# Kernel tuning notes

Hardware: AMD Instinct MI355X
Metric: run time of the kernel (lower is better)

Reference implementation:

```python
import jax, jax.numpy as jnp
import numpy as np

B, I, N, D = 4, 32, 4096, 64
TEM = 1.0
WP = 0.5


def setup_inputs() -> dict:
    key = jax.random.key(0)
    kf, kl = jax.random.split(key)
    x = jax.random.normal(kf, (B, N, D), dtype=jnp.float32)
    # features are L2-normalized ('normed_corr_features')
    x = x / jnp.linalg.norm(x, axis=-1, keepdims=True)
    # assign each correspondence to one of I instances -> boolean masks [B, I, N]
    inst = jax.random.randint(kl, (B, N), 0, I)
    label = (inst[:, None, :] == jnp.arange(I)[None, :, None])  # bool [B, I, N]
    return {"normed_corr_features": x, "label": label}


def reference(normed_corr_features, label):
    x = normed_corr_features                      # [B, N, D]
    m = label.astype(x.dtype)                     # [B, I, N]
    cnt = m.sum(-1)                               # [B, I]
    valid = (cnt >= 5).astype(x.dtype)            # skip instances with <5 points

    sim = jnp.einsum('bpd,bnd->bpn', x, x)        # [B, N, N] full similarity

    # loss_p: mse(sim_p, ones) over the cnt x cnt masked submatrix
    sq = (sim - 1.0) ** 2                         # [B, N, N]
    t = jnp.einsum('bip,bpn->bin', m, sq)         # [B, I, N]
    lp = (t * m).sum(-1) / jnp.maximum(cnt * cnt, 1.0)  # [B, I]

    # loss_n: mean over positive rows p of log(sum over negatives n of exp(sim/tem))
    e = jnp.exp(sim / TEM)                        # [B, N, N]
    s = jnp.einsum('bpn,bin->bip', e, 1.0 - m)    # [B, I, N] row sums over negatives
    ln = (jnp.log(jnp.maximum(s, 1e-30)) * m).sum(-1) / jnp.maximum(cnt, 1.0)  # [B, I]

    denom = jnp.asarray(B * I, x.dtype)
    loss_p = (valid * lp).sum() / denom
    loss_n = (valid * ln).sum() / denom
    return WP * loss_p + (1.0 - WP) * loss_n
```

## Files before the change

### kernel.cpp

```cpp
#include <hip/hip_runtime.h>
#include <stdint.h>

#define Bsz 4
#define Isz 32
#define Nsz 4096
#define Dsz 64
#define WPc 0.5f
#define ALPHA 1.2011224087864498f
#define LN2 0.69314718055994531f
#define LSZ2 256
#define GBLK (Isz * Bsz * 2)

typedef __attribute__((ext_vector_type(8))) short short8;
typedef __attribute__((ext_vector_type(4))) float floatx4;

__device__ inline uint16_t f2bf(float f) {
  uint32_t u = __float_as_uint(f);
  u += 0x7fffu + ((u >> 16) & 1u);
  return (uint16_t)(u >> 16);
}
__device__ inline float exp2_raw(float f) { return __builtin_amdgcn_exp2f(f); }

__device__ inline void load_lds16(const uint16_t* g, void* l) {
  __builtin_amdgcn_global_load_lds(
      (const __attribute__((address_space(1))) uint32_t*)g,
      (__attribute__((address_space(3))) uint32_t*)l, 16, 0, 0);
}

__global__ __launch_bounds__(256) void prep_kernel(
    const float* __restrict__ x, uint16_t* __restrict__ xb,
    float* __restrict__ negtot, float* __restrict__ accum,
    int* __restrict__ ticket) {
  const int t = threadIdx.x;
  const int blk = blockIdx.x;
  const int idx4 = (blk * 256 + t) * 4;
  const float4 v = *(const float4*)(x + idx4);
  ushort4 o;
  o.x = f2bf(v.x * ALPHA);
  o.y = f2bf(v.y * ALPHA);
  o.z = f2bf(v.z * ALPHA);
  o.w = f2bf(v.w * ALPHA);
  *(ushort4*)(xb + idx4) = o;
  if (blk < 64) {
    const int p = blk * 256 + t;
    negtot[p] = 0.f;
    if (p == 0) {
      accum[0] = 0.f;
      ticket[0] = 0;
    }
  }
}

__global__ __launch_bounds__(256) void rowsum4_kernel(
    const uint16_t* __restrict__ xb, float* __restrict__ negtot) {
  __shared__ uint4 sbuf[2][1024];

  const int t = threadIdx.x;
  const int lane = t & 63;
  const int w = t >> 6;
  const int quad = lane >> 4;
  const int l15 = lane & 15;

  const int b = blockIdx.y;
  const int row0 = (blockIdx.x >> 3) * 128;
  const int cg0 = (blockIdx.x & 7) * 512;
  const size_t bN = (size_t)b * Nsz;
  const uint16_t* xbB = xb + bN * Dsz;
  const int wrow0 = row0 + w * 32;

  short8 af[2][2];
#pragma unroll
  for (int rt = 0; rt < 2; ++rt)
#pragma unroll
    for (int kh = 0; kh < 2; ++kh)
      af[rt][kh] = *(const short8*)(xbB + (size_t)(wrow0 + rt * 16 + l15) * Dsz +
                                    quad * 8 + kh * 32);

  float negAll[2][4] = {{0.f, 0.f, 0.f, 0.f}, {0.f, 0.f, 0.f, 0.f}};

#pragma unroll
  for (int k = 0; k < 4; ++k) {
    const int S = w * 256 + k * 64 + lane;
    const int col = S >> 3;
    const int u = (S & 7) ^ (col & 7);
    load_lds16(xbB + (size_t)(cg0 + col) * Dsz + u * 8,
               (void*)((uint4*)sbuf[0] + w * 256 + k * 64));
  }
  __syncthreads();

#pragma unroll
  for (int it = 0; it < 4; ++it) {
    const int cur = it & 1;
    if (it < 3) {
      const int c0 = cg0 + (it + 1) * 128;
#pragma unroll
      for (int k = 0; k < 4; ++k) {
        const int S = w * 256 + k * 64 + lane;
        const int col = S >> 3;
        const int u = (S & 7) ^ (col & 7);
        load_lds16(xbB + (size_t)(c0 + col) * Dsz + u * 8,
                   (void*)((uint4*)sbuf[cur ^ 1] + w * 256 + k * 64));
      }
    }
#pragma unroll
    for (int h = 0; h < 2; ++h) {
      short8 bf[4][2];
#pragma unroll
      for (int ci = 0; ci < 4; ++ci) {
        const int col = (h * 4 + ci) * 16 + l15;
#pragma unroll
        for (int kh = 0; kh < 2; ++kh) {
          const int u = quad + kh * 4;
          bf[ci][kh] = *(const short8*)&sbuf[cur][(col << 3) | (u ^ (col & 7))];
        }
      }
      floatx4 acc[2][4];
#pragma unroll
      for (int rt = 0; rt < 2; ++rt)
#pragma unroll
        for (int ci = 0; ci < 4; ++ci) acc[rt][ci] = (floatx4){0.f, 0.f, 0.f, 0.f};
#pragma unroll
      for (int kh = 0; kh < 2; ++kh)
#pragma unroll
        for (int ci = 0; ci < 4; ++ci)
#pragma unroll
          for (int rt = 0; rt < 2; ++rt)
            acc[rt][ci] = __builtin_amdgcn_mfma_f32_16x16x32_bf16(
                af[rt][kh], bf[ci][kh], acc[rt][ci], 0, 0, 0);
#pragma unroll
      for (int ci = 0; ci < 4; ++ci)
#pragma unroll
        for (int rt = 0; rt < 2; ++rt)
#pragma unroll
          for (int r = 0; r < 4; ++r) negAll[rt][r] += exp2_raw(acc[rt][ci][r]);
    }
    __syncthreads();
  }

#pragma unroll
  for (int rt = 0; rt < 2; ++rt)
#pragma unroll
    for (int r = 0; r < 4; ++r) {
      float g = negAll[rt][r];
#pragma unroll
      for (int m = 1; m < 16; m <<= 1) g += __shfl_xor(g, m, 64);
      if (l15 == 0)
        atomicAdd(&negtot[bN + wrow0 + rt * 16 + quad * 4 + r], g);
    }
}

__global__ __launch_bounds__(256) void gram2_kernel(
    const uint16_t* __restrict__ xb, const uint8_t* __restrict__ label,
    const float* __restrict__ negtot, float* __restrict__ accum,
    int* __restrict__ ticket, float* __restrict__ out) {
  __shared__ int list[LSZ2];
  __shared__ int scnt;
  __shared__ uint4 grow[LSZ2 * 8];
  __shared__ float sPos[4];
  __shared__ float sLn[4];

  const int t = threadIdx.x;
  const int lane = t & 63;
  const int w = t >> 6;
  const int quad = lane >> 4;
  const int l15 = lane & 15;
  const int i = blockIdx.x;
  const int b = blockIdx.y;
  const int rc = blockIdx.z;
  const size_t bN = (size_t)b * Nsz;
  const uint16_t* xbB = xb + bN * Dsz;

  if (t == 0) scnt = 0;
  __syncthreads();
  {
    const uint4 lv = ((const uint4*)(label + ((size_t)b * Isz + i) * Nsz))[t];
    const uint32_t words[4] = {lv.x, lv.y, lv.z, lv.w};
#pragma unroll
    for (int jw = 0; jw < 4; ++jw)
#pragma unroll
      for (int jb = 0; jb < 4; ++jb) {
        if ((words[jw] >> (jb * 8)) & 0xff) {
          const int idx = atomicAdd(&scnt, 1);
          if (idx < LSZ2) list[idx] = t * 16 + jw * 4 + jb;
        }
      }
  }
  __syncthreads();
  const int cnt = scnt;
  const int cntE = cnt < LSZ2 ? cnt : LSZ2;

  for (int s = t; s < cntE * 8; s += 256) {
    const int j = s >> 3, u = s & 7;
    grow[(j << 3) | (u ^ (j & 7))] =
        *(const uint4*)(xbB + (size_t)list[j] * Dsz + u * 8);
  }
  __syncthreads();

  const bool active = (cnt >= 5) && (rc * 128 < cntE);
  if (active) {
    short8 af[2][2];
#pragma unroll
    for (int rt = 0; rt < 2; ++rt) {
      int ridx = rc * 128 + w * 32 + rt * 16 + l15;
      ridx = ridx < cntE ? ridx : cntE - 1;
#pragma unroll
      for (int kh = 0; kh < 2; ++kh) {
        const int u = quad + kh * 4;
        af[rt][kh] = *(const short8*)&grow[(ridx << 3) | (u ^ (ridx & 7))];
      }
    }

    float pos = 0.f, lns = 0.f;
    float ngrow_acc[2][4] = {{0.f, 0.f, 0.f, 0.f}, {0.f, 0.f, 0.f, 0.f}};
    const int nch = (cntE + 127) >> 7;
    for (int cc = 0; cc < nch; ++cc) {
      short8 bfr[8][2];
      bool cvalid[8];
#pragma unroll
      for (int ct = 0; ct < 8; ++ct) {
        const int cidx0 = cc * 128 + ct * 16 + l15;
        const int cidx = cidx0 < cntE ? cidx0 : cntE - 1;
        cvalid[ct] = cidx0 < cntE;
#pragma unroll
        for (int kh = 0; kh < 2; ++kh) {
          const int u = quad + kh * 4;
          bfr[ct][kh] = *(const short8*)&grow[(cidx << 3) | (u ^ (cidx & 7))];
        }
      }
      floatx4 acc[2][8];
#pragma unroll
      for (int rt = 0; rt < 2; ++rt)
#pragma unroll
        for (int ct = 0; ct < 8; ++ct) acc[rt][ct] = (floatx4){0.f, 0.f, 0.f, 0.f};
#pragma unroll
      for (int kh = 0; kh < 2; ++kh)
#pragma unroll
        for (int ct = 0; ct < 8; ++ct)
#pragma unroll
          for (int rt = 0; rt < 2; ++rt)
            acc[rt][ct] = __builtin_amdgcn_mfma_f32_16x16x32_bf16(
                af[rt][kh], bfr[ct][kh], acc[rt][ct], 0, 0, 0);
#pragma unroll
      for (int rt = 0; rt < 2; ++rt) {
        const int rbase = rc * 128 + w * 32 + rt * 16 + quad * 4;
#pragma unroll
        for (int ct = 0; ct < 8; ++ct) {
#pragma unroll
          for (int r = 0; r < 4; ++r) {
            const bool ok = cvalid[ct] && (rbase + r < cntE);
            const float s = acc[rt][ct][r];
            const float d = __builtin_fmaf(s, LN2, -1.f);
            pos += ok ? d * d : 0.f;
            ngrow_acc[rt][r] += ok ? exp2_raw(s) : 0.f;
          }
        }
      }
    }
#pragma unroll
    for (int rt = 0; rt < 2; ++rt)
#pragma unroll
      for (int r = 0; r < 4; ++r) {
        float g = ngrow_acc[rt][r];
#pragma unroll
        for (int m = 1; m < 16; m <<= 1) g += __shfl_xor(g, m, 64);
        const int ridx = rc * 128 + w * 32 + rt * 16 + quad * 4 + r;
        if (l15 == 0 && ridx < cntE) {
          const float nf = negtot[bN + list[ridx]] - g;
          lns += __logf(fmaxf(nf, 1e-30f));
        }
      }
#pragma unroll
    for (int m = 1; m < 64; m <<= 1) {
      pos += __shfl_xor(pos, m, 64);
      lns += __shfl_xor(lns, m, 64);
    }
    if (lane == 0) {
      sPos[w] = pos;
      sLn[w] = lns;
    }
    __syncthreads();
    if (t == 0) {
      const float pt = sPos[0] + sPos[1] + sPos[2] + sPos[3];
      const float lt = sLn[0] + sLn[1] + sLn[2] + sLn[3];
      const float c = (float)cnt;
      atomicAdd(accum, WPc * pt / (c * c) + (1.f - WPc) * lt / c);
    }
  }
  if (t == 0) {
    __threadfence();
    const int old = atomicAdd(ticket, 1);
    if (old == GBLK - 1) {
      const float tot = atomicAdd(accum, 0.f);
      out[0] = tot / (float)(Bsz * Isz);
    }
  }
}

extern "C" void kernel_launch(void* const* d_in, const int* in_sizes, int n_in,
                              void* d_out, int out_size, void* d_ws,
                              size_t ws_size, hipStream_t stream) {
  const float* x = (const float*)d_in[0];
  const uint8_t* label = (const uint8_t*)d_in[1];
  float* out = (float*)d_out;

  uint16_t* xb = (uint16_t*)d_ws;
  float* negtot = (float*)(xb + (size_t)Bsz * Nsz * Dsz);
  float* accum = negtot + Bsz * Nsz;
  int* ticket = (int*)(accum + 1);

  prep_kernel<<<(Bsz * Nsz * Dsz) / (256 * 4), 256, 0, stream>>>(
      x, xb, negtot, accum, ticket);

  dim3 gridA(256, Bsz);
  rowsum4_kernel<<<gridA, 256, 0, stream>>>(xb, negtot);

  dim3 gridB(Isz, Bsz, 2);
  gram2_kernel<<<gridB, 256, 0, stream>>>(xb, label, negtot, accum, ticket, out);
}
```

Before: 92.47 us.

## Prepack bf16 features into MFMA fragment layout and drop LDS staging in rowsum

The prep kernel now also writes a second copy of the bf16 features, pre-arranged so that each 16-row tile's MFMA operand fragments are contiguous per lane. The rowsum kernel drops its double-buffered LDS staging and barriers and instead loads B fragments straight from global memory with fully coalesced 16-byte loads, relying on L2 for reuse. This removes LDS traffic and syncs but makes the rowsum loop depend on global-load latency with no explicit prefetch, and prep writes an extra copy.

```diff
diff --git a/kernel.cpp b/kernel.cpp
--- a/kernel.cpp
+++ b/kernel.cpp
@@ -21,16 +21,10 @@
 }
 __device__ inline float exp2_raw(float f) { return __builtin_amdgcn_exp2f(f); }
 
-__device__ inline void load_lds16(const uint16_t* g, void* l) {
-  __builtin_amdgcn_global_load_lds(
-      (const __attribute__((address_space(1))) uint32_t*)g,
-      (__attribute__((address_space(3))) uint32_t*)l, 16, 0, 0);
-}
-
 __global__ __launch_bounds__(256) void prep_kernel(
     const float* __restrict__ x, uint16_t* __restrict__ xb,
-    float* __restrict__ negtot, float* __restrict__ accum,
-    int* __restrict__ ticket) {
+    uint4* __restrict__ xbf, float* __restrict__ negtot,
+    float* __restrict__ accum, int* __restrict__ ticket) {
   const int t = threadIdx.x;
   const int blk = blockIdx.x;
   const int idx4 = (blk * 256 + t) * 4;
@@ -41,6 +35,26 @@
   o.z = f2bf(v.z * ALPHA);
   o.w = f2bf(v.w * ALPHA);
   *(ushort4*)(xb + idx4) = o;
+
+  if (blk < 512) {
+    const int gid = blk * 256 + t;
+    const int lane = gid & 63;
+    const int kh = (gid >> 6) & 1;
+    const int tile_g = gid >> 7;
+    const int m = lane & 15;
+    const int quad = lane >> 4;
+    const size_t src = (size_t)(tile_g * 16 + m) * Dsz + kh * 32 + quad * 8;
+    const float4 a = *(const float4*)(x + src);
+    const float4 c = *(const float4*)(x + src + 4);
+    ushort4 lo, hi;
+    lo.x = f2bf(a.x * ALPHA); lo.y = f2bf(a.y * ALPHA);
+    lo.z = f2bf(a.z * ALPHA); lo.w = f2bf(a.w * ALPHA);
+    hi.x = f2bf(c.x * ALPHA); hi.y = f2bf(c.y * ALPHA);
+    hi.z = f2bf(c.z * ALPHA); hi.w = f2bf(c.w * ALPHA);
+    ushort4* dst = (ushort4*)(xbf + gid);
+    dst[0] = lo;
+    dst[1] = hi;
+  }
   if (blk < 64) {
     const int p = blk * 256 + t;
     negtot[p] = 0.f;
@@ -51,10 +65,8 @@
   }
 }
 
-__global__ __launch_bounds__(256) void rowsum4_kernel(
-    const uint16_t* __restrict__ xb, float* __restrict__ negtot) {
-  __shared__ uint4 sbuf[2][1024];
-
+__global__ __launch_bounds__(256) void rowsum5_kernel(
+    const uint4* __restrict__ xbf, float* __restrict__ negtot) {
   const int t = threadIdx.x;
   const int lane = t & 63;
   const int w = t >> 6;
@@ -62,81 +74,54 @@
   const int l15 = lane & 15;
 
   const int b = blockIdx.y;
-  const int row0 = (blockIdx.x >> 3) * 128;
-  const int cg0 = (blockIdx.x & 7) * 512;
+  const int rt0 = (blockIdx.x >> 3) * 8;
+  const int ct0 = (blockIdx.x & 7) * 32;
+  const int tb = b * 256;
+
+  short8 af[2][2];
+#pragma unroll
+  for (int rt = 0; rt < 2; ++rt) {
+    const int tile = tb + rt0 + w * 2 + rt;
+#pragma unroll
+    for (int kh = 0; kh < 2; ++kh)
+      af[rt][kh] = *(const short8*)&xbf[(size_t)(tile * 2 + kh) * 64 + lane];
+  }
+
+  float negAll[2][4] = {{0.f, 0.f, 0.f, 0.f}, {0.f, 0.f, 0.f, 0.f}};
+
+#pragma unroll 1
+  for (int cg = 0; cg < 8; ++cg) {
+    short8 bf[4][2];
+#pragma unroll
+    for (int ci = 0; ci < 4; ++ci) {
+      const int tile = tb + ct0 + cg * 4 + ci;
+#pragma unroll
+      for (int kh = 0; kh < 2; ++kh)
+        bf[ci][kh] = *(const short8*)&xbf[(size_t)(tile * 2 + kh) * 64 + lane];
+    }
+    floatx4 acc[2][4];
+#pragma unroll
+    for (int rt = 0; rt < 2; ++rt)
+#pragma unroll
+      for (int ci = 0; ci < 4; ++ci) acc[rt][ci] = (floatx4){0.f, 0.f, 0.f, 0.f};
+#pragma unroll
+    for (int kh = 0; kh < 2; ++kh)
+#pragma unroll
+      for (int ci = 0; ci < 4; ++ci)
+#pragma unroll
+        for (int rt = 0; rt < 2; ++rt)
+          acc[rt][ci] = __builtin_amdgcn_mfma_f32_16x16x32_bf16(
+              af[rt][kh], bf[ci][kh], acc[rt][ci], 0, 0, 0);
+#pragma unroll
+    for (int ci = 0; ci < 4; ++ci)
+#pragma unroll
+      for (int rt = 0; rt < 2; ++rt)
+#pragma unroll
+        for (int r = 0; r < 4; ++r) negAll[rt][r] += exp2_raw(acc[rt][ci][r]);
+  }
+
   const size_t bN = (size_t)b * Nsz;
-  const uint16_t* xbB = xb + bN * Dsz;
-  const int wrow0 = row0 + w * 32;
-
-  short8 af[2][2];
-#pragma unroll
-  for (int rt = 0; rt < 2; ++rt)
-#pragma unroll
-    for (int kh = 0; kh < 2; ++kh)
-      af[rt][kh] = *(const short8*)(xbB + (size_t)(wrow0 + rt * 16 + l15) * Dsz +
-                                    quad * 8 + kh * 32);
-
-  float negAll[2][4] = {{0.f, 0.f, 0.f, 0.f}, {0.f, 0.f, 0.f, 0.f}};
-
-#pragma unroll
-  for (int k = 0; k < 4; ++k) {
-    const int S = w * 256 + k * 64 + lane;
-    const int col = S >> 3;
-    const int u = (S & 7) ^ (col & 7);
-    load_lds16(xbB + (size_t)(cg0 + col) * Dsz + u * 8,
-               (void*)((uint4*)sbuf[0] + w * 256 + k * 64));
-  }
-  __syncthreads();
-
-#pragma unroll
-  for (int it = 0; it < 4; ++it) {
-    const int cur = it & 1;
-    if (it < 3) {
-      const int c0 = cg0 + (it + 1) * 128;
-#pragma unroll
-      for (int k = 0; k < 4; ++k) {
-        const int S = w * 256 + k * 64 + lane;
-        const int col = S >> 3;
-        const int u = (S & 7) ^ (col & 7);
-        load_lds16(xbB + (size_t)(c0 + col) * Dsz + u * 8,
-                   (void*)((uint4*)sbuf[cur ^ 1] + w * 256 + k * 64));
-      }
-    }
-#pragma unroll
-    for (int h = 0; h < 2; ++h) {
-      short8 bf[4][2];
-#pragma unroll
-      for (int ci = 0; ci < 4; ++ci) {
-        const int col = (h * 4 + ci) * 16 + l15;
-#pragma unroll
-        for (int kh = 0; kh < 2; ++kh) {
-          const int u = quad + kh * 4;
-          bf[ci][kh] = *(const short8*)&sbuf[cur][(col << 3) | (u ^ (col & 7))];
-        }
-      }
-      floatx4 acc[2][4];
-#pragma unroll
-      for (int rt = 0; rt < 2; ++rt)
-#pragma unroll
-        for (int ci = 0; ci < 4; ++ci) acc[rt][ci] = (floatx4){0.f, 0.f, 0.f, 0.f};
-#pragma unroll
-      for (int kh = 0; kh < 2; ++kh)
-#pragma unroll
-        for (int ci = 0; ci < 4; ++ci)
-#pragma unroll
-          for (int rt = 0; rt < 2; ++rt)
-            acc[rt][ci] = __builtin_amdgcn_mfma_f32_16x16x32_bf16(
-                af[rt][kh], bf[ci][kh], acc[rt][ci], 0, 0, 0);
-#pragma unroll
-      for (int ci = 0; ci < 4; ++ci)
-#pragma unroll
-        for (int rt = 0; rt < 2; ++rt)
-#pragma unroll
-          for (int r = 0; r < 4; ++r) negAll[rt][r] += exp2_raw(acc[rt][ci][r]);
-    }
-    __syncthreads();
-  }
-
+  const int wrow0 = rt0 * 16 + w * 32;
 #pragma unroll
   for (int rt = 0; rt < 2; ++rt)
 #pragma unroll
@@ -304,15 +289,16 @@
   float* out = (float*)d_out;
 
   uint16_t* xb = (uint16_t*)d_ws;
-  float* negtot = (float*)(xb + (size_t)Bsz * Nsz * Dsz);
+  uint4* xbf = (uint4*)(xb + (size_t)Bsz * Nsz * Dsz);
+  float* negtot = (float*)(xbf + (size_t)Bsz * Nsz * Dsz / 8);
   float* accum = negtot + Bsz * Nsz;
   int* ticket = (int*)(accum + 1);
 
   prep_kernel<<<(Bsz * Nsz * Dsz) / (256 * 4), 256, 0, stream>>>(
-      x, xb, negtot, accum, ticket);
+      x, xb, xbf, negtot, accum, ticket);
 
   dim3 gridA(256, Bsz);
-  rowsum4_kernel<<<gridA, 256, 0, stream>>>(xb, negtot);
+  rowsum5_kernel<<<gridA, 256, 0, stream>>>(xbf, negtot);
 
   dim3 gridB(Isz, Bsz, 2);
   gram2_kernel<<<gridB, 256, 0, stream>>>(xb, label, negtot, accum, ticket, out);
```

After: 89.09 us. 3.6% less time.
